# Kernel tuning notes

Hardware: AMD Instinct MI355X
Metric: run time of the kernel (lower is better)

Reference implementation:

```python
import jax, jax.numpy as jnp
import numpy as np


def setup_inputs() -> dict:
    key = jax.random.key(0)
    k1, k2, k3, k4 = jax.random.split(key, 4)
    B, D_IN, D, N, A = 32, 2048, 128, 400000, 7
    return {
        "x": jax.random.normal(k1, (B, D_IN), dtype=jnp.float32),
        "W_enc": jax.random.normal(k2, (D_IN, D), dtype=jnp.float32) * 0.02,
        "b_enc": jnp.zeros((D,), dtype=jnp.float32),
        "reps": jax.random.normal(k3, (N, D), dtype=jnp.float32),
        "actions": jax.random.normal(k4, (N, A), dtype=jnp.float32),
        "k": 5,
    }


def reference(x, W_enc, b_enc, reps, actions, k):
    # encoder embed: [B, D]
    batch_rep = x @ W_enc + b_enc
    # euclidean cdist: [B, N]
    sq = (
        jnp.sum(batch_rep * batch_rep, axis=-1, keepdims=True)
        + jnp.sum(reps * reps, axis=-1)[None, :]
        - 2.0 * (batch_rep @ reps.T)
    )
    dists = jnp.sqrt(jnp.maximum(sq, 1e-12))
    # top-k smallest distances
    neg_topk, indices = jax.lax.top_k(-dists, k)  # [B, k]
    top_k_distances = -neg_topk
    # gather actions: [B, k, A]
    top_k_actions = actions[indices]
    # softmax(-distance) weights: [B, k]
    weights = jax.nn.softmax(-top_k_distances, axis=1)
    # weighted average: [B, A]
    pred = jnp.sum(top_k_actions * weights[..., None], axis=1)
    return pred
```

## Files before the change

kernel.cpp:

```cpp
#include <hip/hip_runtime.h>
#include <math.h>

#define BATCH 32
#define DIN   2048
#define DK    128
#define NREPS 400000
#define ACT   7
#define NGRP2 3125
#define GBLK  782

__device__ __forceinline__ void topk_insert(float s, int n,
    float& d0, float& d1, float& d2, float& d3, float& d4,
    int& i0, int& i1, int& i2, int& i3, int& i4)
{
    if (s < d4) {
        if (s < d3) {
            d4 = d3; i4 = i3;
            if (s < d2) {
                d3 = d2; i3 = i2;
                if (s < d1) {
                    d2 = d1; i2 = i1;
                    if (s < d0) { d1 = d0; i1 = i0; d0 = s; i0 = n; }
                    else        { d1 = s;  i1 = n; }
                } else { d2 = s; i2 = n; }
            } else { d3 = s; i3 = n; }
        } else { d4 = s; i4 = n; }
    }
}

__global__ __launch_bounds__(256) void encoder_kernel(
    const float* __restrict__ x, const float* __restrict__ W,
    const float* __restrict__ be, float* __restrict__ brept,
    float* __restrict__ brnorm)
{
    __shared__ float xs[DIN];
    __shared__ float part[256];
    __shared__ float vrow[DK];
    const int b = blockIdx.x, t = threadIdx.x;

    const float4* x4 = (const float4*)(x + (size_t)b * DIN);
    float4* xs4 = (float4*)xs;
    xs4[t]       = x4[t];
    xs4[t + 256] = x4[t + 256];
    __syncthreads();

    const int d = t & 127, hh = t >> 7;
    const float* Wp = W + (size_t)(hh * 1024) * DK + d;
    const float* xp = xs + hh * 1024;
    float a0 = 0.f, a1 = 0.f, a2 = 0.f, a3 = 0.f;
    for (int i = 0; i < 1024; i += 8) {
        const float w0 = Wp[(size_t)i * DK];
        const float w1 = Wp[(size_t)(i + 1) * DK];
        const float w2 = Wp[(size_t)(i + 2) * DK];
        const float w3 = Wp[(size_t)(i + 3) * DK];
        const float w4 = Wp[(size_t)(i + 4) * DK];
        const float w5 = Wp[(size_t)(i + 5) * DK];
        const float w6 = Wp[(size_t)(i + 6) * DK];
        const float w7 = Wp[(size_t)(i + 7) * DK];
        a0 = fmaf(xp[i],     w0, a0);
        a1 = fmaf(xp[i + 1], w1, a1);
        a2 = fmaf(xp[i + 2], w2, a2);
        a3 = fmaf(xp[i + 3], w3, a3);
        a0 = fmaf(xp[i + 4], w4, a0);
        a1 = fmaf(xp[i + 5], w5, a1);
        a2 = fmaf(xp[i + 6], w6, a2);
        a3 = fmaf(xp[i + 7], w7, a3);
    }
    part[t] = (a0 + a1) + (a2 + a3);
    __syncthreads();
    if (t < DK) {
        float v = part[t] + part[t + 128] + be[t];
        brept[t * BATCH + b] = -2.0f * v;
        vrow[t] = v * v;
    }
    __syncthreads();
    if (t == 0) {
        float s = 0.f;
        for (int i = 0; i < DK; i++) s += vrow[i];
        brnorm[b] = s;
    }
}

#define FMA4(Acc, S) \
    Acc.x = fmaf(p0.x, S.x, Acc.x); Acc.x = fmaf(p1.x, S.y, Acc.x); \
    Acc.x = fmaf(p2.x, S.z, Acc.x); Acc.x = fmaf(p3.x, S.w, Acc.x); \
    Acc.y = fmaf(p0.y, S.x, Acc.y); Acc.y = fmaf(p1.y, S.y, Acc.y); \
    Acc.y = fmaf(p2.y, S.z, Acc.y); Acc.y = fmaf(p3.y, S.w, Acc.y); \
    Acc.z = fmaf(p0.z, S.x, Acc.z); Acc.z = fmaf(p1.z, S.y, Acc.z); \
    Acc.z = fmaf(p2.z, S.z, Acc.z); Acc.z = fmaf(p3.z, S.w, Acc.z); \
    Acc.w = fmaf(p0.w, S.x, Acc.w); Acc.w = fmaf(p1.w, S.y, Acc.w); \
    Acc.w = fmaf(p2.w, S.z, Acc.w); Acc.w = fmaf(p3.w, S.w, Acc.w);

__global__ __launch_bounds__(256, 2) void dist_topk_kernel(
    const float* __restrict__ reps, const float* __restrict__ brt,
    float* __restrict__ pd, int* __restrict__ pi)
{
    __shared__ float sbrt[DK * BATCH];
    __shared__ float wdist[4 * 64 * 36];
    const int t = threadIdx.x, blk = blockIdx.x;
    const int wid = t >> 6, ln = t & 63;
    const int b = ln & 31, h = ln >> 5;
    float* wd = wdist + wid * (64 * 36);

    {
        const float4* bsrc = (const float4*)brt;
        float4* bdst = (float4*)sbrt;
        #pragma unroll
        for (int i = 0; i < 4; i++) bdst[t + 256 * i] = bsrc[t + 256 * i];
    }
    __syncthreads();

    float d0 = 3.0e38f, d1 = 3.0e38f, d2 = 3.0e38f, d3 = 3.0e38f, d4 = 3.0e38f;
    int   i0 = 0, i1 = 0, i2 = 0, i3 = 0, i4 = 0;

    const float4* sb4 = (const float4*)sbrt;
    const int g = blk * 4 + wid;

    if (g < NGRP2) {
        const float4* rp0 = (const float4*)(reps + (size_t)(g * 128 + ln) * DK);
        const float4* rp1 = rp0 + 64 * (DK / 4);

        float4 a0[8], a1[8];
        #pragma unroll
        for (int q = 0; q < 8; q++) {
            a0[q] = make_float4(0.f, 0.f, 0.f, 0.f);
            a1[q] = make_float4(0.f, 0.f, 0.f, 0.f);
        }
        float n0 = 0.f, n1 = 0.f;

        #pragma unroll 1
        for (int c = 0; c < 4; c++) {
            float4 s0 = rp0[c * 8];
            float4 s1 = rp1[c * 8];
            #pragma unroll
            for (int q = 0; q < 8; q++) {
                float4 t0, t1;
                if (q < 7) { t0 = rp0[c * 8 + q + 1]; t1 = rp1[c * 8 + q + 1]; }
                n0 = fmaf(s0.x, s0.x, n0); n0 = fmaf(s0.y, s0.y, n0);
                n0 = fmaf(s0.z, s0.z, n0); n0 = fmaf(s0.w, s0.w, n0);
                n1 = fmaf(s1.x, s1.x, n1); n1 = fmaf(s1.y, s1.y, n1);
                n1 = fmaf(s1.z, s1.z, n1); n1 = fmaf(s1.w, s1.w, n1);
                const float4* pb = sb4 + (c * 32 + q * 4) * 8;
                #pragma unroll
                for (int j = 0; j < 8; j++) {
                    const float4 p0 = pb[j], p1 = pb[j + 8], p2 = pb[j + 16], p3 = pb[j + 24];
                    float4 A = a0[j];
                    FMA4(A, s0)
                    a0[j] = A;
                    float4 B = a1[j];
                    FMA4(B, s1)
                    a1[j] = B;
                }
                if (q < 7) { s0 = t0; s1 = t1; }
            }
        }

        #pragma unroll
        for (int q = 0; q < 8; q++) {
            float4 v = a0[q];
            v.x += n0; v.y += n0; v.z += n0; v.w += n0;
            *(float4*)&wd[ln * 36 + 4 * q] = v;
        }
        asm volatile("s_waitcnt lgkmcnt(0)" ::: "memory");
        {
            const int nb = g * 128;
            #pragma unroll 4
            for (int s = 0; s < 32; s++) {
                const int row = h * 32 + s;
                topk_insert(wd[row * 36 + b], nb + row, d0, d1, d2, d3, d4, i0, i1, i2, i3, i4);
            }
        }
        asm volatile("s_waitcnt lgkmcnt(0)" ::: "memory");

        #pragma unroll
        for (int q = 0; q < 8; q++) {
            float4 v = a1[q];
            v.x += n1; v.y += n1; v.z += n1; v.w += n1;
            *(float4*)&wd[ln * 36 + 4 * q] = v;
        }
        asm volatile("s_waitcnt lgkmcnt(0)" ::: "memory");
        {
            const int nb = g * 128 + 64;
            #pragma unroll 4
            for (int s = 0; s < 32; s++) {
                const int row = h * 32 + s;
                topk_insert(wd[row * 36 + b], nb + row, d0, d1, d2, d3, d4, i0, i1, i2, i3, i4);
            }
        }
        asm volatile("s_waitcnt lgkmcnt(0)" ::: "memory");
    }

    __syncthreads();
    float* cD = wdist;
    int*   cI = (int*)(wdist + 1280);
    {
        const int base = t * 5;
        cD[base]     = d0; cI[base]     = i0;
        cD[base + 1] = d1; cI[base + 1] = i1;
        cD[base + 2] = d2; cI[base + 2] = i2;
        cD[base + 3] = d3; cI[base + 3] = i3;
        cD[base + 4] = d4; cI[base + 4] = i4;
    }
    __syncthreads();
    if (t < 32) {
        float e0 = 3.0e38f, e1 = 3.0e38f, e2 = 3.0e38f, e3 = 3.0e38f, e4 = 3.0e38f;
        int   j0 = 0, j1 = 0, j2 = 0, j3 = 0, j4 = 0;
        for (int j = 0; j < 8; j++) {
            const int base = (t + 32 * j) * 5;
            #pragma unroll
            for (int e = 0; e < 5; e++)
                topk_insert(cD[base + e], cI[base + e],
                            e0, e1, e2, e3, e4, j0, j1, j2, j3, j4);
        }
        const int ob = (blk * BATCH + t) * 5;
        pd[ob] = e0; pd[ob + 1] = e1; pd[ob + 2] = e2; pd[ob + 3] = e3; pd[ob + 4] = e4;
        pi[ob] = j0; pi[ob + 1] = j1; pi[ob + 2] = j2; pi[ob + 3] = j3; pi[ob + 4] = j4;
    }
}

__global__ __launch_bounds__(256) void final_kernel(
    const float* __restrict__ pd, const int* __restrict__ pi,
    const float* __restrict__ brnorm, const float* __restrict__ actions,
    float* __restrict__ out, int G)
{
    __shared__ float lD[256 * 5];
    __shared__ int   lI[256 * 5];
    __shared__ float sD[32 * 5];
    __shared__ int   sI[32 * 5];
    const int b = blockIdx.x, t = threadIdx.x;

    float d0 = 3.0e38f, d1 = 3.0e38f, d2 = 3.0e38f, d3 = 3.0e38f, d4 = 3.0e38f;
    int   i0 = 0, i1 = 0, i2 = 0, i3 = 0, i4 = 0;
    for (int g = t; g < G; g += 256) {
        const int base = (g * BATCH + b) * 5;
        #pragma unroll
        for (int e = 0; e < 5; e++)
            topk_insert(pd[base + e], pi[base + e],
                        d0, d1, d2, d3, d4, i0, i1, i2, i3, i4);
    }
    lD[t * 5] = d0; lD[t * 5 + 1] = d1; lD[t * 5 + 2] = d2; lD[t * 5 + 3] = d3; lD[t * 5 + 4] = d4;
    lI[t * 5] = i0; lI[t * 5 + 1] = i1; lI[t * 5 + 2] = i2; lI[t * 5 + 3] = i3; lI[t * 5 + 4] = i4;
    __syncthreads();
    if (t < 32) {
        d0 = d1 = d2 = d3 = d4 = 3.0e38f; i0 = i1 = i2 = i3 = i4 = 0;
        for (int s = 0; s < 8; s++) {
            const int base = (t * 8 + s) * 5;
            #pragma unroll
            for (int e = 0; e < 5; e++)
                topk_insert(lD[base + e], lI[base + e],
                            d0, d1, d2, d3, d4, i0, i1, i2, i3, i4);
        }
        sD[t * 5] = d0; sD[t * 5 + 1] = d1; sD[t * 5 + 2] = d2; sD[t * 5 + 3] = d3; sD[t * 5 + 4] = d4;
        sI[t * 5] = i0; sI[t * 5 + 1] = i1; sI[t * 5 + 2] = i2; sI[t * 5 + 3] = i3; sI[t * 5 + 4] = i4;
    }
    __syncthreads();
    if (t == 0) {
        d0 = d1 = d2 = d3 = d4 = 3.0e38f; i0 = i1 = i2 = i3 = i4 = 0;
        for (int s = 0; s < 32; s++) {
            const int base = s * 5;
            #pragma unroll
            for (int e = 0; e < 5; e++)
                topk_insert(sD[base + e], sI[base + e],
                            d0, d1, d2, d3, d4, i0, i1, i2, i3, i4);
        }
        const float bn = brnorm[b];
        float dist[5]; int idx[5];
        dist[0] = d0; dist[1] = d1; dist[2] = d2; dist[3] = d3; dist[4] = d4;
        idx[0] = i0; idx[1] = i1; idx[2] = i2; idx[3] = i3; idx[4] = i4;
        float dmin = 3.0e38f;
        #pragma unroll
        for (int e = 0; e < 5; e++) {
            dist[e] = sqrtf(fmaxf(dist[e] + bn, 1e-12f));
            dmin = fminf(dmin, dist[e]);
        }
        float w[5], wsum = 0.f;
        #pragma unroll
        for (int e = 0; e < 5; e++) { w[e] = expf(dmin - dist[e]); wsum += w[e]; }
        const float inv = 1.0f / wsum;
        for (int a = 0; a < ACT; a++) {
            float o = 0.f;
            #pragma unroll
            for (int e = 0; e < 5; e++)
                o = fmaf(w[e], actions[(size_t)idx[e] * ACT + a], o);
            out[b * ACT + a] = o * inv;
        }
    }
}

extern "C" void kernel_launch(void* const* d_in, const int* in_sizes, int n_in,
                              void* d_out, int out_size, void* d_ws, size_t ws_size,
                              hipStream_t stream)
{
    (void)in_sizes; (void)n_in; (void)out_size;
    const float* x       = (const float*)d_in[0];
    const float* W       = (const float*)d_in[1];
    const float* be      = (const float*)d_in[2];
    const float* reps    = (const float*)d_in[3];
    const float* actions = (const float*)d_in[4];

    float* ws     = (float*)d_ws;
    float* brept  = ws;
    float* brnorm = ws + 4096;
    float* pd     = ws + 4160;

    int G = GBLK;
    {
        const size_t avail_f = ws_size / 4;
        if (avail_f < 4160 + (size_t)G * 320) {
            long fit = ((long)avail_f - 4160) / 320;
            G = (fit < 1) ? 1 : (int)fit;
            if (G > GBLK) G = GBLK;
        }
    }
    int* pi = (int*)(pd + (size_t)G * BATCH * 5);

    encoder_kernel  <<<32, 256, 0, stream>>>(x, W, be, brept, brnorm);
    dist_topk_kernel<<<G,  256, 0, stream>>>(reps, brept, pd, pi);
    final_kernel    <<<32, 256, 0, stream>>>(pd, pi, brnorm, actions, (float*)d_out, G);
}
```

Baseline: 528.3 us.

## Stream reps through double-buffered LDS with async global_load_lds prefetch

Each wave no longer loads its rep rows straight into registers with a one-step software prefetch. It now issues asynchronous global-to-LDS loads (`global_load_lds`, 16 bytes per lane) into a per-wave double buffer. The next 16-column slice is staged while the current slice is consumed, with explicit `vmcnt` waits. The goal is to hide global memory latency and free registers in the distance loop. The cost is much more LDS per block: 64 KB of staging plus the 16 KB `sbrt`, which just fits two blocks per CU. The top-k scratch and the merge buffers are aliased onto the staging area and onto `sbrt`.

```diff
diff --git a/kernel.cpp b/kernel.cpp
--- a/kernel.cpp
+++ b/kernel.cpp
@@ -1,5 +1,6 @@
 #include <hip/hip_runtime.h>
 #include <math.h>
+#include <stdint.h>
 
 #define BATCH 32
 #define DIN   2048
@@ -26,6 +27,13 @@
             } else { d3 = s; i3 = n; }
         } else { d4 = s; i4 = n; }
     }
+}
+
+__device__ __forceinline__ void gload_lds16(const float* g, float* l)
+{
+    __builtin_amdgcn_global_load_lds(
+        (const __attribute__((address_space(1))) void*)g,
+        (__attribute__((address_space(3))) void*)l, 16, 0, 0);
 }
 
 __global__ __launch_bounds__(256) void encoder_kernel(
@@ -91,16 +99,30 @@
     Acc.w = fmaf(p0.w, S.x, Acc.w); Acc.w = fmaf(p1.w, S.y, Acc.w); \
     Acc.w = fmaf(p2.w, S.z, Acc.w); Acc.w = fmaf(p3.w, S.w, Acc.w);
 
+#define STAGE(h, bsel) do {                                         \
+    float* dst_ = swave + (bsel) * 2048;                            \
+    const float* s0p_ = rbase0 + (h) * 16;                          \
+    const float* s1p_ = rbase1 + (h) * 16;                          \
+    gload_lds16(s0p_ + 0,  dst_ + 0 * 256);                         \
+    gload_lds16(s0p_ + 4,  dst_ + 1 * 256);                         \
+    gload_lds16(s0p_ + 8,  dst_ + 2 * 256);                         \
+    gload_lds16(s0p_ + 12, dst_ + 3 * 256);                         \
+    gload_lds16(s1p_ + 0,  dst_ + 4 * 256);                         \
+    gload_lds16(s1p_ + 4,  dst_ + 5 * 256);                         \
+    gload_lds16(s1p_ + 8,  dst_ + 6 * 256);                         \
+    gload_lds16(s1p_ + 12, dst_ + 7 * 256);                         \
+} while (0)
+
 __global__ __launch_bounds__(256, 2) void dist_topk_kernel(
     const float* __restrict__ reps, const float* __restrict__ brt,
     float* __restrict__ pd, int* __restrict__ pi)
 {
     __shared__ float sbrt[DK * BATCH];
-    __shared__ float wdist[4 * 64 * 36];
+    __shared__ float stage[4][4096];
     const int t = threadIdx.x, blk = blockIdx.x;
     const int wid = t >> 6, ln = t & 63;
-    const int b = ln & 31, h = ln >> 5;
-    float* wd = wdist + wid * (64 * 36);
+    const int b = ln & 31, h2 = ln >> 5;
+    float* swave = stage[wid];
 
     {
         const float4* bsrc = (const float4*)brt;
@@ -117,8 +139,8 @@
     const int g = blk * 4 + wid;
 
     if (g < NGRP2) {
-        const float4* rp0 = (const float4*)(reps + (size_t)(g * 128 + ln) * DK);
-        const float4* rp1 = rp0 + 64 * (DK / 4);
+        const float* rbase0 = reps + (size_t)(g * 128 + ln) * DK;
+        const float* rbase1 = rbase0 + 64 * DK;
 
         float4 a0[8], a1[8];
         #pragma unroll
@@ -128,19 +150,27 @@
         }
         float n0 = 0.f, n1 = 0.f;
 
+        STAGE(0, 0);
         #pragma unroll 1
-        for (int c = 0; c < 4; c++) {
-            float4 s0 = rp0[c * 8];
-            float4 s1 = rp1[c * 8];
-            #pragma unroll
-            for (int q = 0; q < 8; q++) {
-                float4 t0, t1;
-                if (q < 7) { t0 = rp0[c * 8 + q + 1]; t1 = rp1[c * 8 + q + 1]; }
+        for (int h = 0; h < 8; h++) {
+            if (h < 7) {
+                STAGE(h + 1, (h + 1) & 1);
+                asm volatile("s_waitcnt vmcnt(8)" ::: "memory");
+            } else {
+                asm volatile("s_waitcnt vmcnt(0)" ::: "memory");
+            }
+            __builtin_amdgcn_sched_barrier(0);
+
+            const float* buf = swave + (h & 1) * 2048;
+            #pragma unroll
+            for (int q = 0; q < 4; q++) {
+                const float4 s0 = *(const float4*)&buf[q * 256 + ln * 4];
+                const float4 s1 = *(const float4*)&buf[(4 + q) * 256 + ln * 4];
                 n0 = fmaf(s0.x, s0.x, n0); n0 = fmaf(s0.y, s0.y, n0);
                 n0 = fmaf(s0.z, s0.z, n0); n0 = fmaf(s0.w, s0.w, n0);
                 n1 = fmaf(s1.x, s1.x, n1); n1 = fmaf(s1.y, s1.y, n1);
                 n1 = fmaf(s1.z, s1.z, n1); n1 = fmaf(s1.w, s1.w, n1);
-                const float4* pb = sb4 + (c * 32 + q * 4) * 8;
+                const float4* pb = sb4 + (h * 16 + q * 4) * 8;
                 #pragma unroll
                 for (int j = 0; j < 8; j++) {
                     const float4 p0 = pb[j], p1 = pb[j + 8], p2 = pb[j + 16], p3 = pb[j + 24];
@@ -151,10 +181,10 @@
                     FMA4(B, s1)
                     a1[j] = B;
                 }
-                if (q < 7) { s0 = t0; s1 = t1; }
             }
         }
 
+        float* wd = swave;
         #pragma unroll
         for (int q = 0; q < 8; q++) {
             float4 v = a0[q];
@@ -166,7 +196,7 @@
             const int nb = g * 128;
             #pragma unroll 4
             for (int s = 0; s < 32; s++) {
-                const int row = h * 32 + s;
+                const int row = h2 * 32 + s;
                 topk_insert(wd[row * 36 + b], nb + row, d0, d1, d2, d3, d4, i0, i1, i2, i3, i4);
             }
         }
@@ -183,7 +213,7 @@
             const int nb = g * 128 + 64;
             #pragma unroll 4
             for (int s = 0; s < 32; s++) {
-                const int row = h * 32 + s;
+                const int row = h2 * 32 + s;
                 topk_insert(wd[row * 36 + b], nb + row, d0, d1, d2, d3, d4, i0, i1, i2, i3, i4);
             }
         }
@@ -191,8 +221,8 @@
     }
 
     __syncthreads();
-    float* cD = wdist;
-    int*   cI = (int*)(wdist + 1280);
+    float* cD = sbrt;
+    int*   cI = (int*)(sbrt + 1280);
     {
         const int base = t * 5;
         cD[base]     = d0; cI[base]     = i0;
```

Result: no change. 531.9 us (+0.7%).
